# Optimization experiments

Hardware: AMD Instinct MI355X
Metric: run time of the kernel (lower is better)

Reference implementation:

```python
import jax, jax.numpy as jnp
import numpy as np

N_EDGES = 262144
N_TRIP = 1048576
D = 128
N_RBF = 6
A_DIM = 49  # n_spher * l_spher
N_BIL = 8


def setup_inputs() -> dict:
    key = jax.random.key(0)
    ks = jax.random.split(key, 16)
    s = lambda fan_in: 1.0 / np.sqrt(fan_in)
    return {
        "m_ji": jax.random.normal(ks[0], (N_EDGES, D), jnp.float32),
        "e_rbf": jax.random.normal(ks[1], (N_EDGES, N_RBF), jnp.float32),
        "a_sbf": jax.random.normal(ks[2], (N_TRIP, A_DIM), jnp.float32),
        "nbr_list": jax.random.randint(ks[3], (N_EDGES, 2), 0, 100000),
        "angle_list": jax.random.randint(ks[4], (N_TRIP, 3), 0, N_EDGES),
        "kj_idx": jax.random.randint(ks[5], (N_TRIP,), 0, N_EDGES),
        "nbr_m_w": jax.random.normal(ks[6], (D, D), jnp.float32) * s(D),
        "nbr_m_b": jnp.zeros((D,), jnp.float32),
        "e_rbf_w": jax.random.normal(ks[7], (N_RBF, D), jnp.float32) * s(N_RBF),
        "a_sbf_w": jax.random.normal(ks[8], (A_DIM, N_BIL), jnp.float32) * s(A_DIM),
        "final_w": jax.random.normal(ks[9], (D, N_BIL, D), jnp.float32) * s(N_BIL * D),
        "m_ji_w": jax.random.normal(ks[10], (D, D), jnp.float32) * s(D),
        "m_ji_b": jnp.zeros((D,), jnp.float32),
        "post_w": jax.random.normal(ks[11], (D, D), jnp.float32) * s(D),
        "post_b": jnp.zeros((D,), jnp.float32),
        "res_w": jax.random.normal(ks[12], (3, 2, D, D), jnp.float32) * s(D),
        "res_b": jnp.zeros((3, 2, D), jnp.float32),
    }


def _residual(x, w2, b2):
    # two Dense(swish) layers + skip
    out = x
    for k in range(2):
        out = jax.nn.silu(out @ w2[k] + b2[k])
    return out + x


def reference(m_ji, e_rbf, a_sbf, nbr_list, angle_list, kj_idx,
              nbr_m_w, nbr_m_b, e_rbf_w, a_sbf_w, final_w,
              m_ji_w, m_ji_b, post_w, post_b, res_w, res_b):
    # DirectedMessage: gather per-triplet edge features
    t_m = jax.nn.silu(m_ji[kj_idx] @ nbr_m_w + nbr_m_b)   # [W, D]
    t_e = e_rbf[kj_idx] @ e_rbf_w                          # [W, D]
    m_and_e = t_m * t_e                                    # [W, D]
    t_a = a_sbf @ a_sbf_w                                  # [W, J]
    out = jnp.einsum('wj,wl,ijl->wi', t_a, m_and_e, final_w)  # [W, D]
    directed = jax.ops.segment_sum(out, kj_idx, num_segments=m_ji.shape[0])  # [E, D]

    transf_m_ji = jax.nn.silu(m_ji @ m_ji_w + m_ji_b)
    output = directed + transf_m_ji
    output = _residual(output, res_w[0], res_b[0])
    output = jax.nn.silu(output @ post_w + post_b) + transf_m_ji
    output = _residual(output, res_w[1], res_b[1])
    output = _residual(output, res_w[2], res_b[2])
    return output
```

## Files before the change

### kernel.cpp

```cpp
#include <hip/hip_runtime.h>

#define N_EDGE 262144
#define N_TRI  1048576
#define DIM    128
#define NRBF   6
#define ADIM   49
#define NBIL   8
#define TE     64
#define NTHR   256
#define SXD    68
#define EB2    2048
#define NSL    4

typedef __attribute__((ext_vector_type(8))) short bf16x8;
typedef __attribute__((ext_vector_type(4))) float f32x4;

__device__ __forceinline__ float fast_rcp(float x) {
    float r; asm("v_rcp_f32 %0, %1" : "=v"(r) : "v"(x)); return r;
}
__device__ __forceinline__ float fast_exp2(float x) {
    float r; asm("v_exp_f32 %0, %1" : "=v"(r) : "v"(x)); return r;
}
__device__ __forceinline__ float silu_f(float x) {
    return x * fast_rcp(1.f + fast_exp2(-1.44269504f * x));
}
__device__ __forceinline__ unsigned short f2bf(float f) {
    unsigned int u = __float_as_uint(f);
    return (unsigned short)((u + 0x7FFFu + ((u >> 16) & 1u)) >> 16);
}
__device__ __forceinline__ unsigned int pk2(float x, float y) {
    unsigned int r;
    asm("v_cvt_pk_bf16_f32 %0, %1, %2" : "=v"(r) : "v"(x), "v"(y));
    return r;
}
__device__ __forceinline__ float bf2f(unsigned short u) {
    return __uint_as_float(((unsigned int)u) << 16);
}

__global__ __launch_bounds__(256) void prep_w_k(
    const float* __restrict__ nbr, const float* __restrict__ mji,
    const float* __restrict__ post, const float* __restrict__ res,
    const float* __restrict__ fw, unsigned short* __restrict__ wt)
{
    int idx = blockIdx.x * 256 + threadIdx.x;
    if (idx < 9 * 16384) {
        int m = idx >> 14, rr = idx & 16383;
        int n = rr >> 7, ks = rr & 127;
        int ko = (ks & ~31) | ((ks & 1) << 4) | ((ks >> 1) & 15);
        const float* src = (m == 0) ? nbr : (m == 1) ? mji : (m == 2) ? post
                          : (res + (size_t)(m - 3) * 16384);
        wt[idx] = f2bf(src[ko * DIM + n]);
    } else {
        int r2 = idx - 9 * 16384;
        int n = r2 >> 10, j = (r2 >> 7) & 7, ls = r2 & 127;
        int lo = (ls & ~31) | ((ls & 1) << 4) | ((ls >> 1) & 15);
        wt[idx] = f2bf(fw[(size_t)(n * NBIL + j) * DIM + lo]);
    }
}

__global__ __launch_bounds__(256) void ta_all_k(
    const float* __restrict__ a_sbf, const float* __restrict__ a_sbf_w,
    float* __restrict__ taw)
{
    __shared__ __align__(16) float sA[256 * ADIM];
    __shared__ float sWa[ADIM * NBIL];
    const int tid = threadIdx.x;
    const size_t w0 = (size_t)blockIdx.x * 256;

    {
        const float4* src = (const float4*)(a_sbf + w0 * ADIM);
        float4* dst = (float4*)sA;
        for (int i = tid; i < (256 * ADIM) / 4; i += 256) dst[i] = src[i];
    }
    for (int i = tid; i < ADIM * NBIL; i += 256) sWa[i] = a_sbf_w[i];
    __syncthreads();

    float ta[NBIL];
    #pragma unroll
    for (int j = 0; j < NBIL; ++j) ta[j] = 0.0f;
    const float* row = sA + tid * ADIM;
    #pragma unroll
    for (int k = 0; k < ADIM; ++k) {
        float v = row[k];
        #pragma unroll
        for (int j = 0; j < NBIL; ++j) ta[j] = fmaf(v, sWa[k * NBIL + j], ta[j]);
    }
    float4* dst = (float4*)(taw + (w0 + tid) * NBIL);
    dst[0] = make_float4(ta[0], ta[1], ta[2], ta[3]);
    dst[1] = make_float4(ta[4], ta[5], ta[6], ta[7]);
}

__global__ __launch_bounds__(1024) void seg_reduce_k(
    const float* __restrict__ taw, const int* __restrict__ kj_idx,
    float* __restrict__ ta_sum)
{
    __shared__ float acc[EB2 * NBIL];
    const int tid = threadIdx.x;
    const int eg = blockIdx.x >> 2;
    const int sl = blockIdx.x & 3;
    const int lo = eg * EB2;

    for (int i = tid; i < EB2 * NBIL; i += 1024) acc[i] = 0.f;
    __syncthreads();

    const int4* kj4 = (const int4*)kj_idx;
    const int i0 = sl * (N_TRI / 4 / NSL);
    const int i1 = i0 + (N_TRI / 4 / NSL);
    for (int i = i0 + tid; i < i1; i += 1024) {
        int4 v = kj4[i];
        int w0 = i * 4;
        #pragma unroll
        for (int k = 0; k < 4; ++k) {
            int e = (k == 0) ? v.x : (k == 1) ? v.y : (k == 2) ? v.z : v.w;
            unsigned d = (unsigned)(e - lo);
            if (d < (unsigned)EB2) {
                const float4* p = (const float4*)(taw + (size_t)(w0 + k) * NBIL);
                float4 a = p[0], b = p[1];
                float* q = acc + d * NBIL;
                atomicAdd(q + 0, a.x); atomicAdd(q + 1, a.y);
                atomicAdd(q + 2, a.z); atomicAdd(q + 3, a.w);
                atomicAdd(q + 4, b.x); atomicAdd(q + 5, b.y);
                atomicAdd(q + 6, b.z); atomicAdd(q + 7, b.w);
            }
        }
    }
    __syncthreads();
    for (int i = tid; i < EB2 * NBIL; i += 1024)
        unsafeAtomicAdd(ta_sum + (size_t)lo * NBIL + i, acc[i]);
}

__global__ __launch_bounds__(256) void triplet_atomic_k(
    const float* __restrict__ a_sbf, const float* __restrict__ a_sbf_w,
    const int* __restrict__ kj_idx, float* __restrict__ ta_sum)
{
    __shared__ __align__(16) float sA[256 * ADIM];
    __shared__ float sWa[ADIM * NBIL];
    const int tid = threadIdx.x;
    const size_t w0 = (size_t)blockIdx.x * 256;
    {
        const float4* src = (const float4*)(a_sbf + w0 * ADIM);
        float4* dst = (float4*)sA;
        for (int i = tid; i < (256 * ADIM) / 4; i += 256) dst[i] = src[i];
    }
    for (int i = tid; i < ADIM * NBIL; i += 256) sWa[i] = a_sbf_w[i];
    __syncthreads();
    float ta[NBIL];
    #pragma unroll
    for (int j = 0; j < NBIL; ++j) ta[j] = 0.0f;
    const float* row = sA + tid * ADIM;
    #pragma unroll
    for (int k = 0; k < ADIM; ++k) {
        float v = row[k];
        #pragma unroll
        for (int j = 0; j < NBIL; ++j) ta[j] = fmaf(v, sWa[k * NBIL + j], ta[j]);
    }
    const int e = kj_idx[w0 + tid];
    float* dst = ta_sum + (size_t)e * NBIL;
    #pragma unroll
    for (int j = 0; j < NBIL; ++j) unsafeAtomicAdd(dst + j, ta[j]);
}

__global__ __launch_bounds__(NTHR) void edge_main_k(
    const float* __restrict__ m_ji, const float* __restrict__ e_rbf,
    const float* __restrict__ ta_sum, const unsigned short* __restrict__ wt,
    const float* __restrict__ nbr_m_b, const float* __restrict__ e_rbf_w,
    const float* __restrict__ m_ji_b, const float* __restrict__ post_b,
    const float* __restrict__ res_b, float* __restrict__ out)
{
    __shared__ __align__(16) unsigned int sXd[2][TE * SXD];
    __shared__ __align__(16) float sTAT[NBIL * TE];
    __shared__ __align__(16) float sET[NRBF * TE];

    const int tid  = threadIdx.x;
    const int lane = tid & 63;
    const int ml   = lane & 15;
    const int g    = lane >> 4;
    const int wq   = tid >> 6;
    const int n0   = wq * 32;
    const int q16  = wq * 16;
    const size_t e0 = (size_t)blockIdx.x * TE;

    unsigned int* tscr = (unsigned int*)(out + e0 * DIM);

    bf16x8 A[4][2], Bf[2][4];
    f32x4 acc[4][2], xr[4][2], bs0, bs1;

    auto prefB = [&](const unsigned short* wtm, int ldk, int kbase) {
        #pragma unroll
        for (int nt = 0; nt < 2; ++nt) {
            const unsigned short* wb =
                wtm + (size_t)(n0 + nt * 16 + ml) * ldk + kbase + g * 8;
            #pragma unroll
            for (int ks = 0; ks < 4; ++ks)
                Bf[nt][ks] = *(const bf16x8*)(wb + ks * 32);
        }
    };
    auto ldbias = [&](const float* bp) {
        float b0 = bp[n0 + ml], b1 = bp[n0 + 16 + ml];
        bs0[0] = b0; bs0[1] = b0; bs0[2] = b0; bs0[3] = b0;
        bs1[0] = b1; bs1[1] = b1; bs1[2] = b1; bs1[3] = b1;
    };
    auto ldzero = [&]() {
        #pragma unroll
        for (int r = 0; r < 4; ++r) { bs0[r] = 0.f; bs1[r] = 0.f; }
    };

    prefB(wt + 1 * 16384, DIM, 0);

    #pragma unroll
    for (int i = 0; i < 4; ++i) {
        int q = tid + i * NTHR;
        int row = q >> 4, sub = q & 15;
        int dq = sub >> 2, c4 = (sub & 3) * 4;
        const float* src = m_ji + (e0 + row) * DIM + dq * 32 + c4;
        float4 a = *(const float4*)(src);
        float4 b = *(const float4*)(src + 16);
        uint4 d;
        d.x = pk2(a.x, b.x); d.y = pk2(a.y, b.y);
        d.z = pk2(a.z, b.z); d.w = pk2(a.w, b.w);
        *(uint4*)(sXd[0] + row * SXD + dq * 16 + c4) = d;
    }
    #pragma unroll
    for (int i = 0; i < 2; ++i) {
        int idx = tid + i * NTHR;
        int j = idx >> 6, e = idx & 63;
        sTAT[j * TE + e] = ta_sum[(e0 + e) * NBIL + j];
    }
    for (int i = tid; i < NRBF * TE; i += NTHR) {
        int j = i >> 6, e = i & 63;
        sET[j * TE + e] = e_rbf[(e0 + e) * NRBF + j];
    }
    __syncthreads();

    auto loadA = [&](const unsigned int* bufp, int h) {
        const unsigned short* base = (const unsigned short*)bufp;
        #pragma unroll
        for (int mt = 0; mt < 4; ++mt) {
            const unsigned short* rb = base + (mt * 16 + ml) * (SXD * 2) + h * 64 + g * 8;
            A[mt][0] = *(const bf16x8*)(rb);
            A[mt][1] = *(const bf16x8*)(rb + 32);
        }
    };
    auto mfmaH = [&](int h, bool seed) {
        #pragma unroll
        for (int kk = 0; kk < 2; ++kk)
        #pragma unroll
        for (int nt = 0; nt < 2; ++nt)
        #pragma unroll
        for (int mt = 0; mt < 4; ++mt) {
            f32x4 cin = (seed && kk == 0) ? (nt == 0 ? bs0 : bs1) : acc[mt][nt];
            acc[mt][nt] = __builtin_amdgcn_mfma_f32_16x16x32_bf16(
                A[mt][kk], Bf[nt][h * 2 + kk], cin, 0, 0, 0);
        }
    };
    auto gemm_full = [&](const unsigned int* bufp) {
        loadA(bufp, 0); mfmaH(0, true); loadA(bufp, 1); mfmaH(1, false);
    };
    auto store_sX = [&](unsigned int* bufp, f32x4 (&v)[4][2]) {
        #pragma unroll
        for (int mt = 0; mt < 4; ++mt)
        #pragma unroll
        for (int r = 0; r < 4; ++r)
            bufp[(mt * 16 + g * 4 + r) * SXD + q16 + ml] = pk2(v[mt][0][r], v[mt][1][r]);
        __syncthreads();
    };

    unsigned int* bufA = sXd[0];
    unsigned int* bufB = sXd[1];

    ldbias(m_ji_b);
    gemm_full(bufA);
    prefB(wt + 0 * 16384, DIM, 0);
    #pragma unroll
    for (int mt = 0; mt < 4; ++mt)
    #pragma unroll
    for (int r = 0; r < 4; ++r)
        tscr[(mt * 16 + g * 4 + r) * 64 + q16 + ml] =
            pk2(silu_f(acc[mt][0][r]), silu_f(acc[mt][1][r]));

    ldbias(nbr_m_b);
    float ewc[2][NRBF];
    #pragma unroll
    for (int nt = 0; nt < 2; ++nt)
    #pragma unroll
    for (int q = 0; q < NRBF; ++q)
        ewc[nt][q] = e_rbf_w[q * DIM + n0 + nt * 16 + ml];
    gemm_full(bufA);
    const unsigned short* fwb = wt + 9 * 16384;
    prefB(fwb, NBIL * DIM, 0);
    #pragma unroll
    for (int mt = 0; mt < 4; ++mt) {
        f32x4 er[NRBF];
        #pragma unroll
        for (int q = 0; q < NRBF; ++q)
            er[q] = *(const f32x4*)(sET + q * TE + mt * 16 + g * 4);
        #pragma unroll
        for (int r = 0; r < 4; ++r) {
            float te0 = 0.f, te1 = 0.f;
            #pragma unroll
            for (int q = 0; q < NRBF; ++q) {
                te0 = fmaf(er[q][r], ewc[0][q], te0);
                te1 = fmaf(er[q][r], ewc[1][q], te1);
            }
            acc[mt][0][r] = silu_f(acc[mt][0][r]) * te0;
            acc[mt][1][r] = silu_f(acc[mt][1][r]) * te1;
        }
    }
    store_sX(bufB, acc);

    #pragma unroll
    for (int mt = 0; mt < 4; ++mt)
    #pragma unroll
    for (int r = 0; r < 4; ++r) {
        unsigned int t = tscr[(mt * 16 + g * 4 + r) * 64 + q16 + ml];
        xr[mt][0][r] = bf2f((unsigned short)(t & 0xffff));
        xr[mt][1][r] = bf2f((unsigned short)(t >> 16));
    }
    ldzero();
    for (int j = 0; j < NBIL; ++j) {
        gemm_full(bufB);
        if (j < NBIL - 1) prefB(fwb, NBIL * DIM, (j + 1) * DIM);
        else              prefB(wt + 3 * 16384, DIM, 0);
        #pragma unroll
        for (int mt = 0; mt < 4; ++mt) {
            f32x4 tv = *(const f32x4*)(sTAT + j * TE + mt * 16 + g * 4);
            #pragma unroll
            for (int nt = 0; nt < 2; ++nt)
            #pragma unroll
            for (int r = 0; r < 4; ++r)
                xr[mt][nt][r] = fmaf(tv[r], acc[mt][nt][r], xr[mt][nt][r]);
        }
    }
    store_sX(bufA, xr);

    ldbias(res_b + 0);
    gemm_full(bufA); prefB(wt + 4 * 16384, DIM, 0);
    #pragma unroll
    for (int mt = 0; mt < 4; ++mt)
    #pragma unroll
    for (int r = 0; r < 4; ++r) {
        acc[mt][0][r] = silu_f(acc[mt][0][r]);
        acc[mt][1][r] = silu_f(acc[mt][1][r]);
    }
    store_sX(bufB, acc);
    ldbias(res_b + 128);
    gemm_full(bufB); prefB(wt + 2 * 16384, DIM, 0);
    #pragma unroll
    for (int mt = 0; mt < 4; ++mt)
    #pragma unroll
    for (int r = 0; r < 4; ++r) {
        xr[mt][0][r] += silu_f(acc[mt][0][r]);
        xr[mt][1][r] += silu_f(acc[mt][1][r]);
    }
    store_sX(bufA, xr);

    ldbias(post_b);
    gemm_full(bufA); prefB(wt + 5 * 16384, DIM, 0);
    #pragma unroll
    for (int mt = 0; mt < 4; ++mt)
    #pragma unroll
    for (int r = 0; r < 4; ++r) {
        unsigned int t = tscr[(mt * 16 + g * 4 + r) * 64 + q16 + ml];
        xr[mt][0][r] = silu_f(acc[mt][0][r]) + bf2f((unsigned short)(t & 0xffff));
        xr[mt][1][r] = silu_f(acc[mt][1][r]) + bf2f((unsigned short)(t >> 16));
    }
    store_sX(bufB, xr);

    ldbias(res_b + 256);
    gemm_full(bufB); prefB(wt + 6 * 16384, DIM, 0);
    #pragma unroll
    for (int mt = 0; mt < 4; ++mt)
    #pragma unroll
    for (int r = 0; r < 4; ++r) {
        acc[mt][0][r] = silu_f(acc[mt][0][r]);
        acc[mt][1][r] = silu_f(acc[mt][1][r]);
    }
    store_sX(bufA, acc);
    ldbias(res_b + 384);
    gemm_full(bufA); prefB(wt + 7 * 16384, DIM, 0);
    #pragma unroll
    for (int mt = 0; mt < 4; ++mt)
    #pragma unroll
    for (int r = 0; r < 4; ++r) {
        xr[mt][0][r] += silu_f(acc[mt][0][r]);
        xr[mt][1][r] += silu_f(acc[mt][1][r]);
    }
    store_sX(bufB, xr);

    ldbias(res_b + 512);
    gemm_full(bufB); prefB(wt + 8 * 16384, DIM, 0);
    #pragma unroll
    for (int mt = 0; mt < 4; ++mt)
    #pragma unroll
    for (int r = 0; r < 4; ++r) {
        acc[mt][0][r] = silu_f(acc[mt][0][r]);
        acc[mt][1][r] = silu_f(acc[mt][1][r]);
    }
    store_sX(bufA, acc);
    ldbias(res_b + 640);
    gemm_full(bufA);
    #pragma unroll
    for (int mt = 0; mt < 4; ++mt)
    #pragma unroll
    for (int r = 0; r < 4; ++r) {
        int row = mt * 16 + g * 4 + r;
        out[(e0 + row) * DIM + n0 + ml]      = silu_f(acc[mt][0][r]) + xr[mt][0][r];
        out[(e0 + row) * DIM + n0 + 16 + ml] = silu_f(acc[mt][1][r]) + xr[mt][1][r];
    }
}

extern "C" void kernel_launch(void* const* d_in, const int* in_sizes, int n_in,
                              void* d_out, int out_size, void* d_ws, size_t ws_size,
                              hipStream_t stream)
{
    (void)in_sizes; (void)n_in; (void)out_size;
    const float* m_ji    = (const float*)d_in[0];
    const float* e_rbf   = (const float*)d_in[1];
    const float* a_sbf   = (const float*)d_in[2];
    const int*   kj_idx  = (const int*)d_in[5];
    const float* nbr_m_w = (const float*)d_in[6];
    const float* nbr_m_b = (const float*)d_in[7];
    const float* e_rbf_w = (const float*)d_in[8];
    const float* a_sbf_w = (const float*)d_in[9];
    const float* final_w = (const float*)d_in[10];
    const float* m_ji_w  = (const float*)d_in[11];
    const float* m_ji_b  = (const float*)d_in[12];
    const float* post_w  = (const float*)d_in[13];
    const float* post_b  = (const float*)d_in[14];
    const float* res_w   = (const float*)d_in[15];
    const float* res_b   = (const float*)d_in[16];
    float* out = (float*)d_out;

    const size_t taB  = (size_t)N_EDGE * NBIL * sizeof(float);
    const size_t wtB  = (size_t)278528 * sizeof(unsigned short);
    const size_t tawB = (size_t)N_TRI * NBIL * sizeof(float);

    float* ta_sum = (float*)d_ws;
    unsigned short* wt = (unsigned short*)((char*)d_ws + taB);
    float* taw = (float*)((char*)d_ws + taB + wtB);

    prep_w_k<<<1088, 256, 0, stream>>>(nbr_m_w, m_ji_w, post_w, res_w, final_w, wt);
    hipMemsetAsync(ta_sum, 0, taB, stream);

    if (ws_size >= taB + wtB + tawB) {
        ta_all_k<<<N_TRI / 256, 256, 0, stream>>>(a_sbf, a_sbf_w, taw);
        seg_reduce_k<<<(N_EDGE / EB2) * NSL, 1024, 0, stream>>>(taw, kj_idx, ta_sum);
    } else {
        triplet_atomic_k<<<N_TRI / 256, 256, 0, stream>>>(a_sbf, a_sbf_w, kj_idx, ta_sum);
    }
    edge_main_k<<<N_EDGE / TE, NTHR, 0, stream>>>(m_ji, e_rbf, ta_sum, wt,
        nbr_m_b, e_rbf_w, m_ji_b, post_b, res_b, out);
}
```

Before: 539.1 us.

## Double edge tile to 128 rows with 8 waves, single LDS buffer, LDS transf scratch

The edge kernel now processes 128 edges per block with 512 threads, split into two 64-row wave groups that share each weight B-fragment load. The ping-pong LDS activation buffer becomes a single buffer guarded by a barrier before and after each store. The transf_m_ji scratch moves from the global output buffer into a dedicated LDS array. This cuts global weight traffic per edge and global scratch round-trips, at the cost of an extra barrier per layer and more LDS per block, which may lower occupancy.

```diff
diff --git a/kernel.cpp b/kernel.cpp
--- a/kernel.cpp
+++ b/kernel.cpp
@@ -6,8 +6,8 @@
 #define NRBF   6
 #define ADIM   49
 #define NBIL   8
-#define TE     64
-#define NTHR   256
+#define TE     128
+#define NTHR   512
 #define SXD    68
 #define EB2    2048
 #define NSL    4
@@ -167,7 +167,8 @@
     const float* __restrict__ m_ji_b, const float* __restrict__ post_b,
     const float* __restrict__ res_b, float* __restrict__ out)
 {
-    __shared__ __align__(16) unsigned int sXd[2][TE * SXD];
+    __shared__ __align__(16) unsigned int sXd[TE * SXD];
+    __shared__ __align__(16) unsigned int sTd[TE * SXD];
     __shared__ __align__(16) float sTAT[NBIL * TE];
     __shared__ __align__(16) float sET[NRBF * TE];
 
@@ -175,25 +176,31 @@
     const int lane = tid & 63;
     const int ml   = lane & 15;
     const int g    = lane >> 4;
-    const int wq   = tid >> 6;
-    const int n0   = wq * 32;
-    const int q16  = wq * 16;
+    const int wid  = tid >> 6;
+    const int mb   = (wid >> 2) * 64;
+    const int n0   = (wid & 3) * 32;
+    const int q16  = (wid & 3) * 16;
     const size_t e0 = (size_t)blockIdx.x * TE;
-
-    unsigned int* tscr = (unsigned int*)(out + e0 * DIM);
 
     bf16x8 A[4][2], Bf[2][4];
     f32x4 acc[4][2], xr[4][2], bs0, bs1;
 
-    auto prefB = [&](const unsigned short* wtm, int ldk, int kbase) {
-        #pragma unroll
-        for (int nt = 0; nt < 2; ++nt) {
-            const unsigned short* wb =
-                wtm + (size_t)(n0 + nt * 16 + ml) * ldk + kbase + g * 8;
-            #pragma unroll
-            for (int ks = 0; ks < 4; ++ks)
-                Bf[nt][ks] = *(const bf16x8*)(wb + ks * 32);
-        }
+    const int offD0 = (n0 + ml) * DIM + g * 8;
+    const int offD1 = (n0 + 16 + ml) * DIM + g * 8;
+    const int offF0 = (n0 + ml) * (NBIL * DIM) + g * 8;
+    const int offF1 = (n0 + 16 + ml) * (NBIL * DIM) + g * 8;
+
+    auto prefB = [&](const unsigned short* wtm, int kbase) {
+        const bf16x8* p0 = (const bf16x8*)(wtm + offD0 + kbase);
+        const bf16x8* p1 = (const bf16x8*)(wtm + offD1 + kbase);
+        #pragma unroll
+        for (int ks = 0; ks < 4; ++ks) { Bf[0][ks] = p0[ks * 4]; Bf[1][ks] = p1[ks * 4]; }
+    };
+    auto prefBF = [&](const unsigned short* wtm, int kbase) {
+        const bf16x8* p0 = (const bf16x8*)(wtm + offF0 + kbase);
+        const bf16x8* p1 = (const bf16x8*)(wtm + offF1 + kbase);
+        #pragma unroll
+        for (int ks = 0; ks < 4; ++ks) { Bf[0][ks] = p0[ks * 4]; Bf[1][ks] = p1[ks * 4]; }
     };
     auto ldbias = [&](const float* bp) {
         float b0 = bp[n0 + ml], b1 = bp[n0 + 16 + ml];
@@ -205,7 +212,7 @@
         for (int r = 0; r < 4; ++r) { bs0[r] = 0.f; bs1[r] = 0.f; }
     };
 
-    prefB(wt + 1 * 16384, DIM, 0);
+    prefB(wt + 1 * 16384, 0);
 
     #pragma unroll
     for (int i = 0; i < 4; ++i) {
@@ -218,25 +225,26 @@
         uint4 d;
         d.x = pk2(a.x, b.x); d.y = pk2(a.y, b.y);
         d.z = pk2(a.z, b.z); d.w = pk2(a.w, b.w);
-        *(uint4*)(sXd[0] + row * SXD + dq * 16 + c4) = d;
+        *(uint4*)(sXd + row * SXD + dq * 16 + c4) = d;
     }
     #pragma unroll
     for (int i = 0; i < 2; ++i) {
         int idx = tid + i * NTHR;
-        int j = idx >> 6, e = idx & 63;
+        int j = idx >> 7, e = idx & 127;
         sTAT[j * TE + e] = ta_sum[(e0 + e) * NBIL + j];
     }
     for (int i = tid; i < NRBF * TE; i += NTHR) {
-        int j = i >> 6, e = i & 63;
+        int j = i >> 7, e = i & 127;
         sET[j * TE + e] = e_rbf[(e0 + e) * NRBF + j];
     }
     __syncthreads();
 
-    auto loadA = [&](const unsigned int* bufp, int h) {
-        const unsigned short* base = (const unsigned short*)bufp;
+    auto loadA = [&](int h) {
+        const unsigned short* base = (const unsigned short*)sXd;
         #pragma unroll
         for (int mt = 0; mt < 4; ++mt) {
-            const unsigned short* rb = base + (mt * 16 + ml) * (SXD * 2) + h * 64 + g * 8;
+            const unsigned short* rb =
+                base + (mb + mt * 16 + ml) * (SXD * 2) + h * 64 + g * 8;
             A[mt][0] = *(const bf16x8*)(rb);
             A[mt][1] = *(const bf16x8*)(rb + 32);
         }
@@ -253,29 +261,26 @@
                 A[mt][kk], Bf[nt][h * 2 + kk], cin, 0, 0, 0);
         }
     };
-    auto gemm_full = [&](const unsigned int* bufp) {
-        loadA(bufp, 0); mfmaH(0, true); loadA(bufp, 1); mfmaH(1, false);
-    };
-    auto store_sX = [&](unsigned int* bufp, f32x4 (&v)[4][2]) {
+    auto gemm_full = [&]() { loadA(0); mfmaH(0, true); loadA(1); mfmaH(1, false); };
+    auto store_sX = [&](f32x4 (&v)[4][2]) {
+        __syncthreads();
         #pragma unroll
         for (int mt = 0; mt < 4; ++mt)
         #pragma unroll
         for (int r = 0; r < 4; ++r)
-            bufp[(mt * 16 + g * 4 + r) * SXD + q16 + ml] = pk2(v[mt][0][r], v[mt][1][r]);
+            sXd[(mb + mt * 16 + g * 4 + r) * SXD + q16 + ml] =
+                pk2(v[mt][0][r], v[mt][1][r]);
         __syncthreads();
     };
 
-    unsigned int* bufA = sXd[0];
-    unsigned int* bufB = sXd[1];
-
     ldbias(m_ji_b);
-    gemm_full(bufA);
-    prefB(wt + 0 * 16384, DIM, 0);
+    gemm_full();
+    prefB(wt + 0 * 16384, 0);
     #pragma unroll
     for (int mt = 0; mt < 4; ++mt)
     #pragma unroll
     for (int r = 0; r < 4; ++r)
-        tscr[(mt * 16 + g * 4 + r) * 64 + q16 + ml] =
+        sTd[(mb + mt * 16 + g * 4 + r) * SXD + q16 + ml] =
             pk2(silu_f(acc[mt][0][r]), silu_f(acc[mt][1][r]));
 
     ldbias(nbr_m_b);
@@ -285,15 +290,15 @@
     #pragma unroll
     for (int q = 0; q < NRBF; ++q)
         ewc[nt][q] = e_rbf_w[q * DIM + n0 + nt * 16 + ml];
-    gemm_full(bufA);
+    gemm_full();
     const unsigned short* fwb = wt + 9 * 16384;
-    prefB(fwb, NBIL * DIM, 0);
+    prefBF(fwb, 0);
     #pragma unroll
     for (int mt = 0; mt < 4; ++mt) {
         f32x4 er[NRBF];
         #pragma unroll
         for (int q = 0; q < NRBF; ++q)
-            er[q] = *(const f32x4*)(sET + q * TE + mt * 16 + g * 4);
+            er[q] = *(const f32x4*)(sET + q * TE + mb + mt * 16 + g * 4);
         #pragma unroll
         for (int r = 0; r < 4; ++r) {
             float te0 = 0.f, te1 = 0.f;
@@ -306,24 +311,24 @@
             acc[mt][1][r] = silu_f(acc[mt][1][r]) * te1;
         }
     }
-    store_sX(bufB, acc);
-
-    #pragma unroll
-    for (int mt = 0; mt < 4; ++mt)
-    #pragma unroll
-    for (int r = 0; r < 4; ++r) {
-        unsigned int t = tscr[(mt * 16 + g * 4 + r) * 64 + q16 + ml];
+    store_sX(acc);
+
+    #pragma unroll
+    for (int mt = 0; mt < 4; ++mt)
+    #pragma unroll
+    for (int r = 0; r < 4; ++r) {
+        unsigned int t = sTd[(mb + mt * 16 + g * 4 + r) * SXD + q16 + ml];
         xr[mt][0][r] = bf2f((unsigned short)(t & 0xffff));
         xr[mt][1][r] = bf2f((unsigned short)(t >> 16));
     }
     ldzero();
     for (int j = 0; j < NBIL; ++j) {
-        gemm_full(bufB);
-        if (j < NBIL - 1) prefB(fwb, NBIL * DIM, (j + 1) * DIM);
-        else              prefB(wt + 3 * 16384, DIM, 0);
+        gemm_full();
+        if (j < NBIL - 1) prefBF(fwb, (j + 1) * DIM);
+        else              prefB(wt + 3 * 16384, 0);
         #pragma unroll
         for (int mt = 0; mt < 4; ++mt) {
-            f32x4 tv = *(const f32x4*)(sTAT + j * TE + mt * 16 + g * 4);
+            f32x4 tv = *(const f32x4*)(sTAT + j * TE + mb + mt * 16 + g * 4);
             #pragma unroll
             for (int nt = 0; nt < 2; ++nt)
             #pragma unroll
@@ -331,10 +336,10 @@
                 xr[mt][nt][r] = fmaf(tv[r], acc[mt][nt][r], xr[mt][nt][r]);
         }
     }
-    store_sX(bufA, xr);
+    store_sX(xr);
 
     ldbias(res_b + 0);
-    gemm_full(bufA); prefB(wt + 4 * 16384, DIM, 0);
+    gemm_full(); prefB(wt + 4 * 16384, 0);
     #pragma unroll
     for (int mt = 0; mt < 4; ++mt)
     #pragma unroll
@@ -342,9 +347,9 @@
         acc[mt][0][r] = silu_f(acc[mt][0][r]);
         acc[mt][1][r] = silu_f(acc[mt][1][r]);
     }
-    store_sX(bufB, acc);
+    store_sX(acc);
     ldbias(res_b + 128);
-    gemm_full(bufB); prefB(wt + 2 * 16384, DIM, 0);
+    gemm_full(); prefB(wt + 2 * 16384, 0);
     #pragma unroll
     for (int mt = 0; mt < 4; ++mt)
     #pragma unroll
@@ -352,22 +357,22 @@
         xr[mt][0][r] += silu_f(acc[mt][0][r]);
         xr[mt][1][r] += silu_f(acc[mt][1][r]);
     }
-    store_sX(bufA, xr);
+    store_sX(xr);
 
     ldbias(post_b);
-    gemm_full(bufA); prefB(wt + 5 * 16384, DIM, 0);
-    #pragma unroll
-    for (int mt = 0; mt < 4; ++mt)
-    #pragma unroll
-    for (int r = 0; r < 4; ++r) {
-        unsigned int t = tscr[(mt * 16 + g * 4 + r) * 64 + q16 + ml];
+    gemm_full(); prefB(wt + 5 * 16384, 0);
+    #pragma unroll
+    for (int mt = 0; mt < 4; ++mt)
+    #pragma unroll
+    for (int r = 0; r < 4; ++r) {
+        unsigned int t = sTd[(mb + mt * 16 + g * 4 + r) * SXD + q16 + ml];
         xr[mt][0][r] = silu_f(acc[mt][0][r]) + bf2f((unsigned short)(t & 0xffff));
         xr[mt][1][r] = silu_f(acc[mt][1][r]) + bf2f((unsigned short)(t >> 16));
     }
-    store_sX(bufB, xr);
+    store_sX(xr);
 
     ldbias(res_b + 256);
-    gemm_full(bufB); prefB(wt + 6 * 16384, DIM, 0);
+    gemm_full(); prefB(wt + 6 * 16384, 0);
     #pragma unroll
     for (int mt = 0; mt < 4; ++mt)
     #pragma unroll
@@ -375,9 +380,9 @@
         acc[mt][0][r] = silu_f(acc[mt][0][r]);
         acc[mt][1][r] = silu_f(acc[mt][1][r]);
     }
-    store_sX(bufA, acc);
+    store_sX(acc);
     ldbias(res_b + 384);
-    gemm_full(bufA); prefB(wt + 7 * 16384, DIM, 0);
+    gemm_full(); prefB(wt + 7 * 16384, 0);
     #pragma unroll
     for (int mt = 0; mt < 4; ++mt)
     #pragma unroll
@@ -385,10 +390,10 @@
         xr[mt][0][r] += silu_f(acc[mt][0][r]);
         xr[mt][1][r] += silu_f(acc[mt][1][r]);
     }
-    store_sX(bufB, xr);
+    store_sX(xr);
 
     ldbias(res_b + 512);
-    gemm_full(bufB); prefB(wt + 8 * 16384, DIM, 0);
+    gemm_full(); prefB(wt + 8 * 16384, 0);
     #pragma unroll
     for (int mt = 0; mt < 4; ++mt)
     #pragma unroll
@@ -396,14 +401,14 @@
         acc[mt][0][r] = silu_f(acc[mt][0][r]);
         acc[mt][1][r] = silu_f(acc[mt][1][r]);
     }
-    store_sX(bufA, acc);
+    store_sX(acc);
     ldbias(res_b + 640);
-    gemm_full(bufA);
-    #pragma unroll
-    for (int mt = 0; mt < 4; ++mt)
-    #pragma unroll
-    for (int r = 0; r < 4; ++r) {
-        int row = mt * 16 + g * 4 + r;
+    gemm_full();
+    #pragma unroll
+    for (int mt = 0; mt < 4; ++mt)
+    #pragma unroll
+    for (int r = 0; r < 4; ++r) {
+        int row = mb + mt * 16 + g * 4 + r;
         out[(e0 + row) * DIM + n0 + ml]      = silu_f(acc[mt][0][r]) + xr[mt][0][r];
         out[(e0 + row) * DIM + n0 + 16 + ml] = silu_f(acc[mt][1][r]) + xr[mt][1][r];
     }
```

New measurement: 826.1 us. 1.53x slower.
